# Kernel optimization log

Measured on AMD Instinct MI355X. Metric: run time of the kernel, lower is better.

## Reference

```python
import jax, jax.numpy as jnp
import numpy as np

B, C, H, W, E, R, TOP_K = 8, 128, 128, 128, 4, 64, 2


def setup_inputs() -> dict:
    key = jax.random.key(0)
    ks = jax.random.split(key, 12)
    s = 0.02
    return {
        "x": jax.random.normal(ks[0], (B, C, H, W), jnp.float32),
        "shared": jax.random.normal(ks[1], (B, C, H, W), jnp.float32),
        # FrequencyEmbedding MLP: Linear(C,2C) -> GELU -> Linear(2C,C)
        "mlp_w1": jax.random.normal(ks[2], (C, 2 * C), jnp.float32) * s,
        "mlp_b1": jnp.zeros((2 * C,), jnp.float32),
        "mlp_w2": jax.random.normal(ks[3], (2 * C, C), jnp.float32) * s,
        "mlp_b2": jnp.zeros((C,), jnp.float32),
        # routing gates: Linear(C,E) on pooled x, Linear(C,E) on freq emb
        "gate_w": jax.random.normal(ks[4], (C, E), jnp.float32) * s,
        "freq_gate_w": jax.random.normal(ks[5], (C, E), jnp.float32) * s,
        # per-expert 1x1 conv weights (ModExpert.proj, expert_layer=Identity)
        "exp_w0": jax.random.normal(ks[6], (E, R, C), jnp.float32) * s,  # dim->rank
        "exp_w1": jax.random.normal(ks[7], (E, R, C), jnp.float32) * s,  # dim->rank (on shared)
        "exp_w2": jax.random.normal(ks[8], (E, C, R), jnp.float32) * s,  # rank->dim
        # AdapterLayer.proj_out 1x1 conv
        "proj_w": jax.random.normal(ks[9], (C, C), jnp.float32) * s,
    }


def reference(x, shared, mlp_w1, mlp_b1, mlp_w2, mlp_b2, gate_w, freq_gate_w,
              exp_w0, exp_w1, exp_w2, proj_w):
    b, c = x.shape[0], x.shape[1]
    # --- FrequencyEmbedding: frozen depthwise high-pass 3x3 -> GELU -> mean(HW) -> MLP ---
    hp = jnp.array([[-1., -1., -1.], [-1., 8., -1.], [-1., -1., -1.]], dtype=x.dtype)
    kern = jnp.broadcast_to(hp, (c, 1, 3, 3))
    h = jax.lax.conv_general_dilated(
        x, kern, window_strides=(1, 1), padding='SAME',
        feature_group_count=c, dimension_numbers=('NCHW', 'OIHW', 'NCHW'))
    h = jax.nn.gelu(h, approximate=False)
    fe = h.mean(axis=(-2, -1))                                    # [B, C]
    fe = jax.nn.gelu(fe @ mlp_w1 + mlp_b1, approximate=False) @ mlp_w2 + mlp_b2
    # --- RoutingFunction (eval / noiseless): softmax -> top-k -> scatter gates ---
    pooled = x.mean(axis=(-2, -1))                                # [B, C]
    logits = pooled @ gate_w + fe @ freq_gate_w                   # [B, E]
    scores = jax.nn.softmax(logits, axis=-1)
    vals, idx = jax.lax.top_k(scores, TOP_K)
    gates = jnp.zeros_like(scores).at[jnp.arange(b)[:, None], idx].set(vals)  # [B, E]
    # --- Experts (dense equivalent of SparseDispatcher gather->expert->scatter-add) ---
    # expert_e(x, shared) = x + W2_e @ ((W0_e @ x) * silu(W1_e @ shared))
    a = jnp.einsum('bchw,erc->berhw', x, exp_w0)                  # [B,E,R,H,W]
    g = jax.nn.silu(jnp.einsum('bchw,erc->berhw', shared, exp_w1))
    y = jnp.einsum('berhw,edr->bedhw', a * g, exp_w2)             # [B,E,C,H,W]
    # gated combine; residual shortcut enters once per selected expert, weighted by gate
    out = jnp.einsum('be,bedhw->bdhw', gates, y) + gates.sum(axis=1)[:, None, None, None] * x
    # --- proj_out 1x1 ---
    return jnp.einsum('bchw,dc->bdhw', out, proj_w)
```

## Files before the change

kernel.cpp:

```cpp
#include <hip/hip_runtime.h>
#include <hip/hip_bf16.h>
#include <math.h>

#define CC   128
#define HWN  16384
#define EE   4
#define RR   64
#define TP   64
#define NT   (HWN / TP)

#define XS_STRIDE 136
#define US_STRIDE 72

typedef __attribute__((ext_vector_type(8))) short short8;
typedef __attribute__((ext_vector_type(4))) float f32x4;

__device__ __forceinline__ unsigned short f2bf(float f) {
    __hip_bfloat16 h = __float2bfloat16(f);
    return *reinterpret_cast<unsigned short*>(&h);
}
__device__ __forceinline__ float gelu_exact(float v) {
    return 0.5f * v * (1.0f + erff(v * 0.7071067811865475f));
}
__device__ __forceinline__ float silu_f(float v) {
    return v / (1.0f + expf(-v));
}

__global__ __launch_bounds__(256) void k_weights(
    const float* __restrict__ proj, const float* __restrict__ w0,
    const float* __restrict__ w1,   const float* __restrict__ w2,
    unsigned short* __restrict__ projb, unsigned short* __restrict__ w0b,
    unsigned short* __restrict__ w1b,   unsigned short* __restrict__ w2pb)
{
    const int bx = blockIdx.x, tid = threadIdx.x;
    if (bx < 128) {
        int i = bx * 256 + tid;
        if (i < CC * CC) projb[i] = f2bf(proj[i]);
        w0b[i] = f2bf(w0[i]);
        w1b[i] = f2bf(w1[i]);
    } else {
        const int bb = bx - 128;
        const int e  = bb >> 5;
        const int d  = ((bb & 31) << 2) + (tid >> 6);
        const int r  = tid & 63;
        const float* pr = proj + d * CC;
        const float* wz = w2 + (size_t)e * CC * RR + r;
        float a0 = 0.f, a1 = 0.f, a2 = 0.f, a3 = 0.f;
        for (int c = 0; c < CC; c += 4) {
            a0 += pr[c+0] * wz[(c+0) * RR];
            a1 += pr[c+1] * wz[(c+1) * RR];
            a2 += pr[c+2] * wz[(c+2) * RR];
            a3 += pr[c+3] * wz[(c+3) * RR];
        }
        w2pb[(e * CC + d) * RR + r] = f2bf((a0 + a1) + (a2 + a3));
    }
}

#define IMS 129
__global__ __launch_bounds__(256) void k_convpool(
    const float* __restrict__ x,
    float* __restrict__ fe0, float* __restrict__ pooled)
{
    __shared__ float img[128 * IMS];
    __shared__ float wred[8];
    const int bc = blockIdx.x, tid = threadIdx.x;
    const float4* g = (const float4*)(x + (size_t)bc * HWN);
    for (int i = tid; i < HWN / 4; i += 256) {
        const int r = i >> 5, cq = (i & 31) << 2;
        float4 v = g[i];
        float* d = img + r * IMS + cq;
        d[0] = v.x; d[1] = v.y; d[2] = v.z; d[3] = v.w;
    }
    __syncthreads();
    const int r  = tid >> 1;
    const int c0 = (tid & 1) << 6;
    const float* rm = img + r * IMS + c0;
    const bool has_t = (r > 0), has_b = (r < 127);
    float sg = 0.f, sx = 0.f;
    for (int j = 0; j < 64; ++j) {
        const int cc = c0 + j;
        const float m  = rm[j];
        float s = ((cc > 0) ? rm[j-1] : 0.f) + ((cc < 127) ? rm[j+1] : 0.f);
        if (has_t) {
            const float* rw = rm - IMS;
            s += rw[j] + ((cc > 0) ? rw[j-1] : 0.f) + ((cc < 127) ? rw[j+1] : 0.f);
        }
        if (has_b) {
            const float* rw = rm + IMS;
            s += rw[j] + ((cc > 0) ? rw[j-1] : 0.f) + ((cc < 127) ? rw[j+1] : 0.f);
        }
        sg += gelu_exact(8.f * m - s);
        sx += m;
    }
    for (int off = 32; off > 0; off >>= 1) {
        sg += __shfl_down(sg, off, 64);
        sx += __shfl_down(sx, off, 64);
    }
    if ((tid & 63) == 0) { wred[tid >> 6] = sg; wred[4 + (tid >> 6)] = sx; }
    __syncthreads();
    if (tid == 0) {
        fe0[bc]    = (wred[0] + wred[1] + wred[2] + wred[3]) * (1.f / 16384.f);
        pooled[bc] = (wred[4] + wred[5] + wred[6] + wred[7]) * (1.f / 16384.f);
    }
}

__global__ __launch_bounds__(256) void k_route(
    const float* __restrict__ fe0, const float* __restrict__ pooled,
    const float* __restrict__ w1, const float* __restrict__ b1,
    const float* __restrict__ w2, const float* __restrict__ b2,
    const float* __restrict__ gw, const float* __restrict__ fgw,
    float* __restrict__ gates, float* __restrict__ gsum)
{
    const int b = blockIdx.x, tid = threadIdx.x;
    __shared__ float hh[256];
    __shared__ float fe[128];
    __shared__ float lg[4];
    {
        const float* f0 = fe0 + b * CC;
        float a[8];
        #pragma unroll
        for (int j = 0; j < 8; ++j) a[j] = 0.f;
        for (int c = 0; c < CC; c += 8)
            #pragma unroll
            for (int j = 0; j < 8; ++j) a[j] += f0[c + j] * w1[(c + j) * 256 + tid];
        float acc = b1[tid] + ((a[0]+a[1]) + (a[2]+a[3])) + ((a[4]+a[5]) + (a[6]+a[7]));
        hh[tid] = gelu_exact(acc);
    }
    __syncthreads();
    if (tid < 128) {
        float a[8];
        #pragma unroll
        for (int j = 0; j < 8; ++j) a[j] = 0.f;
        for (int c = 0; c < 256; c += 8)
            #pragma unroll
            for (int j = 0; j < 8; ++j) a[j] += hh[c + j] * w2[(c + j) * 128 + tid];
        fe[tid] = b2[tid] + ((a[0]+a[1]) + (a[2]+a[3])) + ((a[4]+a[5]) + (a[6]+a[7]));
    }
    __syncthreads();
    if (tid < EE) {
        const float* pl = pooled + b * CC;
        float l0=0.f, l1=0.f, l2=0.f, l3=0.f;
        for (int c = 0; c < CC; c += 4) {
            l0 += pl[c+0] * gw[(c+0) * EE + tid] + fe[c+0] * fgw[(c+0) * EE + tid];
            l1 += pl[c+1] * gw[(c+1) * EE + tid] + fe[c+1] * fgw[(c+1) * EE + tid];
            l2 += pl[c+2] * gw[(c+2) * EE + tid] + fe[c+2] * fgw[(c+2) * EE + tid];
            l3 += pl[c+3] * gw[(c+3) * EE + tid] + fe[c+3] * fgw[(c+3) * EE + tid];
        }
        lg[tid] = (l0 + l1) + (l2 + l3);
    }
    __syncthreads();
    if (tid == 0) {
        float mx = fmaxf(fmaxf(lg[0], lg[1]), fmaxf(lg[2], lg[3]));
        float sc[EE]; float ssum = 0.f;
        for (int e = 0; e < EE; ++e) { sc[e] = expf(lg[e] - mx); ssum += sc[e]; }
        float inv = 1.f / ssum;
        for (int e = 0; e < EE; ++e) sc[e] *= inv;
        int i1 = 0;
        for (int e = 1; e < EE; ++e) if (sc[e] > sc[i1]) i1 = e;
        int i2 = -1;
        for (int e = 0; e < EE; ++e) {
            if (e == i1) continue;
            if (i2 < 0 || sc[e] > sc[i2]) i2 = e;
        }
        for (int e = 0; e < EE; ++e)
            gates[b * EE + e] = (e == i1) ? sc[i1] : (e == i2 ? sc[i2] : 0.f);
        gsum[b] = sc[i1] + sc[i2];
    }
}

__global__ __launch_bounds__(256, 3) void k_experts(
    const float* __restrict__ x, const float* __restrict__ sh,
    const unsigned short* __restrict__ w0b, const unsigned short* __restrict__ w1b,
    const unsigned short* __restrict__ w2pb, const unsigned short* __restrict__ projb,
    const float* __restrict__ gates, const float* __restrict__ gsum,
    float* __restrict__ out)
{
    __shared__ __align__(16) unsigned short xs [TP * XS_STRIDE];
    __shared__ __align__(16) unsigned short shs[TP * XS_STRIDE];
    __shared__ __align__(16) unsigned short us [TP * US_STRIDE];
    const int tid  = threadIdx.x;
    const int b    = blockIdx.x >> 8;
    const int tile = blockIdx.x & (NT - 1);
    const int p0   = tile * TP;

    {
        const int p  = tid & 63;
        const int cb = tid >> 6;
        const float* xp = x  + (size_t)b * CC * HWN + p0 + p;
        const float* sp = sh + (size_t)b * CC * HWN + p0 + p;
        for (int it = 0; it < 4; ++it) {
            const int c0 = it * 32 + cb * 8;
            unsigned short t0[8], t1[8];
            #pragma unroll
            for (int j = 0; j < 8; ++j) t0[j] = f2bf(xp[(size_t)(c0 + j) * HWN]);
            #pragma unroll
            for (int j = 0; j < 8; ++j) t1[j] = f2bf(sp[(size_t)(c0 + j) * HWN]);
            *(uint4*)&xs [p * XS_STRIDE + c0] = *(uint4*)t0;
            *(uint4*)&shs[p * XS_STRIDE + c0] = *(uint4*)t1;
        }
    }
    __syncthreads();

    const int wv = tid >> 6;
    const int ln = tid & 63;
    const int lp = ln & 15;
    const int lq = ln >> 4;

    f32x4 acc[2][4];
    #pragma unroll
    for (int i = 0; i < 2; ++i)
        #pragma unroll
        for (int j = 0; j < 4; ++j) acc[i][j] = (f32x4){0.f, 0.f, 0.f, 0.f};

    {
        const int d0 = wv * 32;
        #pragma unroll
        for (int ks = 0; ks < 4; ++ks) {
            const int k0 = ks * 32 + lq * 8;
            short8 a0 = *(const short8*)&projb[(d0 +      lp) * CC + k0];
            short8 a1 = *(const short8*)&projb[(d0 + 16 + lp) * CC + k0];
            #pragma unroll
            for (int pt = 0; pt < 4; ++pt) {
                short8 bf = *(const short8*)&xs[(pt * 16 + lp) * XS_STRIDE + k0];
                acc[0][pt] = __builtin_amdgcn_mfma_f32_16x16x32_bf16(a0, bf, acc[0][pt], 0, 0, 0);
                acc[1][pt] = __builtin_amdgcn_mfma_f32_16x16x32_bf16(a1, bf, acc[1][pt], 0, 0, 0);
            }
        }
        const float gs = gsum[b];
        #pragma unroll
        for (int i = 0; i < 2; ++i)
            #pragma unroll
            for (int j = 0; j < 4; ++j) acc[i][j] *= gs;
    }

    for (int e = 0; e < EE; ++e) {
        const float ge = gates[b * EE + e];
        if (ge == 0.f) continue;

        f32x4 af[4], gf[4];
        #pragma unroll
        for (int pt = 0; pt < 4; ++pt) { af[pt] = (f32x4){0.f,0.f,0.f,0.f}; gf[pt] = (f32x4){0.f,0.f,0.f,0.f}; }
        const unsigned short* w0e = w0b + (size_t)(e * RR + wv * 16) * CC;
        const unsigned short* w1e = w1b + (size_t)(e * RR + wv * 16) * CC;
        #pragma unroll
        for (int ks = 0; ks < 4; ++ks) {
            const int k0 = ks * 32 + lq * 8;
            short8 a0 = *(const short8*)&w0e[lp * CC + k0];
            short8 a1 = *(const short8*)&w1e[lp * CC + k0];
            #pragma unroll
            for (int pt = 0; pt < 4; ++pt) {
                short8 bx = *(const short8*)&xs [(pt * 16 + lp) * XS_STRIDE + k0];
                short8 bs = *(const short8*)&shs[(pt * 16 + lp) * XS_STRIDE + k0];
                af[pt] = __builtin_amdgcn_mfma_f32_16x16x32_bf16(a0, bx, af[pt], 0, 0, 0);
                gf[pt] = __builtin_amdgcn_mfma_f32_16x16x32_bf16(a1, bs, gf[pt], 0, 0, 0);
            }
        }
        __syncthreads();
        #pragma unroll
        for (int pt = 0; pt < 4; ++pt) {
            unsigned short t[4];
            #pragma unroll
            for (int i = 0; i < 4; ++i)
                t[i] = f2bf(ge * af[pt][i] * silu_f(gf[pt][i]));
            *(uint2*)&us[(pt * 16 + lp) * US_STRIDE + wv * 16 + lq * 4] = *(uint2*)t;
        }
        __syncthreads();
        const unsigned short* w2e = w2pb + (size_t)(e * CC + wv * 32) * RR;
        #pragma unroll
        for (int ks = 0; ks < 2; ++ks) {
            const int k0 = ks * 32 + lq * 8;
            short8 a0 = *(const short8*)&w2e[lp * RR + k0];
            short8 a1 = *(const short8*)&w2e[(16 + lp) * RR + k0];
            #pragma unroll
            for (int pt = 0; pt < 4; ++pt) {
                short8 bu = *(const short8*)&us[(pt * 16 + lp) * US_STRIDE + k0];
                acc[0][pt] = __builtin_amdgcn_mfma_f32_16x16x32_bf16(a0, bu, acc[0][pt], 0, 0, 0);
                acc[1][pt] = __builtin_amdgcn_mfma_f32_16x16x32_bf16(a1, bu, acc[1][pt], 0, 0, 0);
            }
        }
    }

    {
        const int d0 = wv * 32;
        #pragma unroll
        for (int dt = 0; dt < 2; ++dt)
            #pragma unroll
            for (int pt = 0; pt < 4; ++pt) {
                float* ob = out + ((size_t)(b * CC + d0 + dt * 16 + lq * 4)) * HWN + p0 + pt * 16 + lp;
                #pragma unroll
                for (int i = 0; i < 4; ++i)
                    ob[(size_t)i * HWN] = acc[dt][pt][i];
            }
    }
}

extern "C" void kernel_launch(void* const* d_in, const int* in_sizes, int n_in,
                              void* d_out, int out_size, void* d_ws, size_t ws_size,
                              hipStream_t stream) {
    const float* x    = (const float*)d_in[0];
    const float* shr  = (const float*)d_in[1];
    const float* mw1  = (const float*)d_in[2];
    const float* mb1  = (const float*)d_in[3];
    const float* mw2  = (const float*)d_in[4];
    const float* mb2  = (const float*)d_in[5];
    const float* gw   = (const float*)d_in[6];
    const float* fgw  = (const float*)d_in[7];
    const float* ew0  = (const float*)d_in[8];
    const float* ew1  = (const float*)d_in[9];
    const float* ew2  = (const float*)d_in[10];
    const float* pw   = (const float*)d_in[11];
    float* out = (float*)d_out;

    float* ws     = (float*)d_ws;
    float* fe0    = ws + 0;
    float* pooled = ws + 1024;
    float* gates  = ws + 2048;
    float* gsum   = ws + 2080;
    unsigned short* projb = (unsigned short*)(ws + 2112);
    unsigned short* w0b   = projb + 16384;
    unsigned short* w1b   = w0b + 32768;
    unsigned short* w2pb  = w1b + 32768;

    k_weights <<<256,     256, 0, stream>>>(pw, ew0, ew1, ew2, projb, w0b, w1b, w2pb);
    k_convpool<<<8 * CC,  256, 0, stream>>>(x, fe0, pooled);
    k_route   <<<8,       256, 0, stream>>>(fe0, pooled, mw1, mb1, mw2, mb2, gw, fgw, gates, gsum);
    k_experts <<<8 * NT,  256, 0, stream>>>(x, shr, w0b, w1b, w2pb, projb, gates, gsum, out);
}
```

Before: 278.3 us.

## Merge prep kernels, prefetch shared into cache, XOR-swizzle LDS, raise occupancy

Merges the weight-conversion and conv/pool kernels into one prep kernel. That kernel also gains extra blocks that stream the whole `shared` tensor and the MLP and gate weights, writing to a dummy only on a value match, so the data sits in the last-level cache before the expert kernel runs. The depthwise stencil now keeps a sliding register window and a zero pad row instead of per-element boundary branches. The expert kernel replaces padded LDS strides with XOR swizzles and raises launch bounds to 4 blocks per CU. The prefetch spends extra memory bandwidth and relies on the cache holding a 64 MB tensor between kernels.

```diff
diff --git a/kernel.cpp b/kernel.cpp
--- a/kernel.cpp
+++ b/kernel.cpp
@@ -9,9 +9,6 @@
 #define TP   64
 #define NT   (HWN / TP)
 
-#define XS_STRIDE 136
-#define US_STRIDE 72
-
 typedef __attribute__((ext_vector_type(8))) short short8;
 typedef __attribute__((ext_vector_type(4))) float f32x4;
 
@@ -26,81 +23,112 @@
     return v / (1.0f + expf(-v));
 }
 
-__global__ __launch_bounds__(256) void k_weights(
-    const float* __restrict__ proj, const float* __restrict__ w0,
-    const float* __restrict__ w1,   const float* __restrict__ w2,
+#define IMS 129
+#define PREP_CONV 1024
+#define PREP_WCV  (PREP_CONV + 128)
+#define PREP_WF   (PREP_WCV + 128)
+#define PREP_SHW  (PREP_WF + 512)
+#define PREP_MLW  (PREP_SHW + 48)
+__global__ __launch_bounds__(256) void k_prep(
+    const float* __restrict__ x,   const float* __restrict__ sh,
+    const float* __restrict__ proj,
+    const float* __restrict__ ew0, const float* __restrict__ ew1,
+    const float* __restrict__ ew2,
+    const float* __restrict__ mw1, const float* __restrict__ mw2,
+    const float* __restrict__ gw,  const float* __restrict__ fgw,
+    float* __restrict__ fe0, float* __restrict__ pooled,
     unsigned short* __restrict__ projb, unsigned short* __restrict__ w0b,
-    unsigned short* __restrict__ w1b,   unsigned short* __restrict__ w2pb)
+    unsigned short* __restrict__ w1b,   unsigned short* __restrict__ w2pb,
+    float* __restrict__ dummy)
 {
+    __shared__ float img[129 * IMS];
+    __shared__ float wred[8];
     const int bx = blockIdx.x, tid = threadIdx.x;
-    if (bx < 128) {
-        int i = bx * 256 + tid;
+
+    if (bx < PREP_CONV) {
+        const int bc = bx;
+        const float4* g = (const float4*)(x + (size_t)bc * HWN);
+        for (int i = tid; i < HWN / 4; i += 256) {
+            const int r = i >> 5, cq = (i & 31) << 2;
+            float4 v = g[i];
+            float* d = img + r * IMS + cq;
+            d[0] = v.x; d[1] = v.y; d[2] = v.z; d[3] = v.w;
+        }
+        for (int i = tid; i < IMS; i += 256) img[128 * IMS + i] = 0.f;
+        __syncthreads();
+
+        const int r  = tid >> 1;
+        const int c0 = (tid & 1) << 6;
+        const float* pm  = img + r * IMS + c0;
+        const float* pt_ = img + ((r > 0)   ? (r - 1) : 128) * IMS + c0;
+        const float* pb_ = img + ((r < 127) ? (r + 1) : 128) * IMS + c0;
+        float l0, l1, l2, m0, m1, m2;
+        if (c0 == 0) { l0 = l1 = l2 = 0.f; }
+        else         { l0 = pt_[-1]; l1 = pm[-1]; l2 = pb_[-1]; }
+        m0 = pt_[0]; m1 = pm[0]; m2 = pb_[0];
+        float sg = 0.f, sx = 0.f;
+        #pragma unroll 7
+        for (int j = 0; j < 63; ++j) {
+            float n0 = pt_[j + 1], n1 = pm[j + 1], n2 = pb_[j + 1];
+            float s8 = ((l0 + l1 + l2) + (m0 + m2)) + ((n0 + n1) + n2);
+            sg += gelu_exact(8.f * m1 - s8);
+            sx += m1;
+            l0 = m0; l1 = m1; l2 = m2; m0 = n0; m1 = n1; m2 = n2;
+        }
+        {
+            float n0, n1, n2;
+            if (c0 == 64) { n0 = n1 = n2 = 0.f; }
+            else          { n0 = pt_[64]; n1 = pm[64]; n2 = pb_[64]; }
+            float s8 = ((l0 + l1 + l2) + (m0 + m2)) + ((n0 + n1) + n2);
+            sg += gelu_exact(8.f * m1 - s8);
+            sx += m1;
+        }
+        for (int off = 32; off > 0; off >>= 1) {
+            sg += __shfl_down(sg, off, 64);
+            sx += __shfl_down(sx, off, 64);
+        }
+        if ((tid & 63) == 0) { wred[tid >> 6] = sg; wred[4 + (tid >> 6)] = sx; }
+        __syncthreads();
+        if (tid == 0) {
+            fe0[bc]    = (wred[0] + wred[1] + wred[2] + wred[3]) * (1.f / 16384.f);
+            pooled[bc] = (wred[4] + wred[5] + wred[6] + wred[7]) * (1.f / 16384.f);
+        }
+    } else if (bx < PREP_WCV) {
+        int i = (bx - PREP_CONV) * 256 + tid;
         if (i < CC * CC) projb[i] = f2bf(proj[i]);
-        w0b[i] = f2bf(w0[i]);
-        w1b[i] = f2bf(w1[i]);
-    } else {
-        const int bb = bx - 128;
+        w0b[i] = f2bf(ew0[i]);
+        w1b[i] = f2bf(ew1[i]);
+    } else if (bx < PREP_WF) {
+        const int bb = bx - PREP_WCV;
         const int e  = bb >> 5;
         const int d  = ((bb & 31) << 2) + (tid >> 6);
         const int r  = tid & 63;
         const float* pr = proj + d * CC;
-        const float* wz = w2 + (size_t)e * CC * RR + r;
+        const float* wz = ew2 + (size_t)e * CC * RR + r;
         float a0 = 0.f, a1 = 0.f, a2 = 0.f, a3 = 0.f;
         for (int c = 0; c < CC; c += 4) {
-            a0 += pr[c+0] * wz[(c+0) * RR];
-            a1 += pr[c+1] * wz[(c+1) * RR];
-            a2 += pr[c+2] * wz[(c+2) * RR];
-            a3 += pr[c+3] * wz[(c+3) * RR];
+            a0 += pr[c + 0] * wz[(c + 0) * RR];
+            a1 += pr[c + 1] * wz[(c + 1) * RR];
+            a2 += pr[c + 2] * wz[(c + 2) * RR];
+            a3 += pr[c + 3] * wz[(c + 3) * RR];
         }
         w2pb[(e * CC + d) * RR + r] = f2bf((a0 + a1) + (a2 + a3));
-    }
-}
-
-#define IMS 129
-__global__ __launch_bounds__(256) void k_convpool(
-    const float* __restrict__ x,
-    float* __restrict__ fe0, float* __restrict__ pooled)
-{
-    __shared__ float img[128 * IMS];
-    __shared__ float wred[8];
-    const int bc = blockIdx.x, tid = threadIdx.x;
-    const float4* g = (const float4*)(x + (size_t)bc * HWN);
-    for (int i = tid; i < HWN / 4; i += 256) {
-        const int r = i >> 5, cq = (i & 31) << 2;
-        float4 v = g[i];
-        float* d = img + r * IMS + cq;
-        d[0] = v.x; d[1] = v.y; d[2] = v.z; d[3] = v.w;
-    }
-    __syncthreads();
-    const int r  = tid >> 1;
-    const int c0 = (tid & 1) << 6;
-    const float* rm = img + r * IMS + c0;
-    const bool has_t = (r > 0), has_b = (r < 127);
-    float sg = 0.f, sx = 0.f;
-    for (int j = 0; j < 64; ++j) {
-        const int cc = c0 + j;
-        const float m  = rm[j];
-        float s = ((cc > 0) ? rm[j-1] : 0.f) + ((cc < 127) ? rm[j+1] : 0.f);
-        if (has_t) {
-            const float* rw = rm - IMS;
-            s += rw[j] + ((cc > 0) ? rw[j-1] : 0.f) + ((cc < 127) ? rw[j+1] : 0.f);
-        }
-        if (has_b) {
-            const float* rw = rm + IMS;
-            s += rw[j] + ((cc > 0) ? rw[j-1] : 0.f) + ((cc < 127) ? rw[j+1] : 0.f);
-        }
-        sg += gelu_exact(8.f * m - s);
-        sx += m;
-    }
-    for (int off = 32; off > 0; off >>= 1) {
-        sg += __shfl_down(sg, off, 64);
-        sx += __shfl_down(sx, off, 64);
-    }
-    if ((tid & 63) == 0) { wred[tid >> 6] = sg; wred[4 + (tid >> 6)] = sx; }
-    __syncthreads();
-    if (tid == 0) {
-        fe0[bc]    = (wred[0] + wred[1] + wred[2] + wred[3]) * (1.f / 16384.f);
-        pooled[bc] = (wred[4] + wred[5] + wred[6] + wred[7]) * (1.f / 16384.f);
+    } else if (bx < PREP_SHW) {
+        const int wb = bx - PREP_WF;
+        const float4* s4 = (const float4*)sh + (size_t)wb * 8192;
+        float s = 0.f;
+        #pragma unroll 4
+        for (int j = 0; j < 32; ++j) {
+            float4 v = s4[j * 256 + tid];
+            s += (v.x + v.y) + (v.z + v.w);
+        }
+        if (s == 12345.678f) dummy[0] = s;
+    } else {
+        const int i = (bx - PREP_SHW) * 256 + tid;
+        float s = 0.f;
+        for (int j = i; j < CC * 2 * CC; j += 48 * 256) s += mw1[j] + mw2[j];
+        if (i < CC * EE) s += gw[i] + fgw[i];
+        if (s == 12345.678f) dummy[1] = s;
     }
 }
 
@@ -168,16 +196,16 @@
     }
 }
 
-__global__ __launch_bounds__(256, 3) void k_experts(
+__global__ __launch_bounds__(256, 4) void k_experts(
     const float* __restrict__ x, const float* __restrict__ sh,
     const unsigned short* __restrict__ w0b, const unsigned short* __restrict__ w1b,
     const unsigned short* __restrict__ w2pb, const unsigned short* __restrict__ projb,
     const float* __restrict__ gates, const float* __restrict__ gsum,
     float* __restrict__ out)
 {
-    __shared__ __align__(16) unsigned short xs [TP * XS_STRIDE];
-    __shared__ __align__(16) unsigned short shs[TP * XS_STRIDE];
-    __shared__ __align__(16) unsigned short us [TP * US_STRIDE];
+    __shared__ __align__(16) unsigned short xs [TP * CC];
+    __shared__ __align__(16) unsigned short shs[TP * CC];
+    __shared__ __align__(16) unsigned short us [TP * RR];
     const int tid  = threadIdx.x;
     const int b    = blockIdx.x >> 8;
     const int tile = blockIdx.x & (NT - 1);
@@ -188,15 +216,17 @@
         const int cb = tid >> 6;
         const float* xp = x  + (size_t)b * CC * HWN + p0 + p;
         const float* sp = sh + (size_t)b * CC * HWN + p0 + p;
+        #pragma unroll
         for (int it = 0; it < 4; ++it) {
             const int c0 = it * 32 + cb * 8;
+            const int sw = p * CC + (((it * 4 + cb) ^ (p & 15)) << 3);
             unsigned short t0[8], t1[8];
             #pragma unroll
             for (int j = 0; j < 8; ++j) t0[j] = f2bf(xp[(size_t)(c0 + j) * HWN]);
             #pragma unroll
             for (int j = 0; j < 8; ++j) t1[j] = f2bf(sp[(size_t)(c0 + j) * HWN]);
-            *(uint4*)&xs [p * XS_STRIDE + c0] = *(uint4*)t0;
-            *(uint4*)&shs[p * XS_STRIDE + c0] = *(uint4*)t1;
+            *(uint4*)&xs [sw] = *(uint4*)t0;
+            *(uint4*)&shs[sw] = *(uint4*)t1;
         }
     }
     __syncthreads();
@@ -217,11 +247,12 @@
         #pragma unroll
         for (int ks = 0; ks < 4; ++ks) {
             const int k0 = ks * 32 + lq * 8;
+            const int ch = ks * 4 + lq;
             short8 a0 = *(const short8*)&projb[(d0 +      lp) * CC + k0];
             short8 a1 = *(const short8*)&projb[(d0 + 16 + lp) * CC + k0];
             #pragma unroll
             for (int pt = 0; pt < 4; ++pt) {
-                short8 bf = *(const short8*)&xs[(pt * 16 + lp) * XS_STRIDE + k0];
+                short8 bf = *(const short8*)&xs[(pt * 16 + lp) * CC + ((ch ^ lp) << 3)];
                 acc[0][pt] = __builtin_amdgcn_mfma_f32_16x16x32_bf16(a0, bf, acc[0][pt], 0, 0, 0);
                 acc[1][pt] = __builtin_amdgcn_mfma_f32_16x16x32_bf16(a1, bf, acc[1][pt], 0, 0, 0);
             }
@@ -245,12 +276,14 @@
         #pragma unroll
         for (int ks = 0; ks < 4; ++ks) {
             const int k0 = ks * 32 + lq * 8;
+            const int ch = ks * 4 + lq;
             short8 a0 = *(const short8*)&w0e[lp * CC + k0];
             short8 a1 = *(const short8*)&w1e[lp * CC + k0];
             #pragma unroll
             for (int pt = 0; pt < 4; ++pt) {
-                short8 bx = *(const short8*)&xs [(pt * 16 + lp) * XS_STRIDE + k0];
-                short8 bs = *(const short8*)&shs[(pt * 16 + lp) * XS_STRIDE + k0];
+                const int sw = (pt * 16 + lp) * CC + ((ch ^ lp) << 3);
+                short8 bx = *(const short8*)&xs [sw];
+                short8 bs = *(const short8*)&shs[sw];
                 af[pt] = __builtin_amdgcn_mfma_f32_16x16x32_bf16(a0, bx, af[pt], 0, 0, 0);
                 gf[pt] = __builtin_amdgcn_mfma_f32_16x16x32_bf16(a1, bs, gf[pt], 0, 0, 0);
             }
@@ -262,18 +295,21 @@
             #pragma unroll
             for (int i = 0; i < 4; ++i)
                 t[i] = f2bf(ge * af[pt][i] * silu_f(gf[pt][i]));
-            *(uint2*)&us[(pt * 16 + lp) * US_STRIDE + wv * 16 + lq * 4] = *(uint2*)t;
+            const int p = pt * 16 + lp;
+            const int addr = p * RR + (((wv * 2 + (lq >> 1)) ^ (lp & 7)) << 3) + ((lq & 1) << 2);
+            *(uint2*)&us[addr] = *(uint2*)t;
         }
         __syncthreads();
         const unsigned short* w2e = w2pb + (size_t)(e * CC + wv * 32) * RR;
         #pragma unroll
         for (int ks = 0; ks < 2; ++ks) {
             const int k0 = ks * 32 + lq * 8;
+            const int ch = ks * 4 + lq;
             short8 a0 = *(const short8*)&w2e[lp * RR + k0];
             short8 a1 = *(const short8*)&w2e[(16 + lp) * RR + k0];
             #pragma unroll
             for (int pt = 0; pt < 4; ++pt) {
-                short8 bu = *(const short8*)&us[(pt * 16 + lp) * US_STRIDE + k0];
+                short8 bu = *(const short8*)&us[(pt * 16 + lp) * RR + ((ch ^ (lp & 7)) << 3)];
                 acc[0][pt] = __builtin_amdgcn_mfma_f32_16x16x32_bf16(a0, bu, acc[0][pt], 0, 0, 0);
                 acc[1][pt] = __builtin_amdgcn_mfma_f32_16x16x32_bf16(a1, bu, acc[1][pt], 0, 0, 0);
             }
@@ -316,13 +352,14 @@
     float* pooled = ws + 1024;
     float* gates  = ws + 2048;
     float* gsum   = ws + 2080;
+    float* dummy  = ws + 2088;
     unsigned short* projb = (unsigned short*)(ws + 2112);
     unsigned short* w0b   = projb + 16384;
     unsigned short* w1b   = w0b + 32768;
     unsigned short* w2pb  = w1b + 32768;
 
-    k_weights <<<256,     256, 0, stream>>>(pw, ew0, ew1, ew2, projb, w0b, w1b, w2pb);
-    k_convpool<<<8 * CC,  256, 0, stream>>>(x, fe0, pooled);
-    k_route   <<<8,       256, 0, stream>>>(fe0, pooled, mw1, mb1, mw2, mb2, gw, fgw, gates, gsum);
-    k_experts <<<8 * NT,  256, 0, stream>>>(x, shr, w0b, w1b, w2pb, projb, gates, gsum, out);
-}
+    k_prep   <<<PREP_MLW, 256, 0, stream>>>(x, shr, pw, ew0, ew1, ew2, mw1, mw2,
+                                            gw, fgw, fe0, pooled, projb, w0b, w1b, w2pb, dummy);
+    k_route  <<<8,        256, 0, stream>>>(fe0, pooled, mw1, mb1, mw2, mb2, gw, fgw, gates, gsum);
+    k_experts<<<8 * NT,   256, 0, stream>>>(x, shr, w0b, w1b, w2pb, projb, gates, gsum, out);
+}
```

After: 259.8 us. 1.07x faster.
